# Kernel optimization log

Hardware: AMD Instinct MI355X
Metric: run time of the kernel (lower is better)

## Reference

```python
import jax, jax.numpy as jnp
import numpy as np

N_NODES = 10000
N_EDGES = 320000
K_HOPS = 3
IN_CH = 128
OUT_CH = 128


def setup_inputs() -> dict:
    key = jax.random.key(0)
    k1, k2, k3, k4, k5 = jax.random.split(key, 5)
    h = jax.random.normal(k1, (N_NODES, IN_CH), dtype=jnp.float32)
    X = jax.random.normal(k2, (N_EDGES, K_HOPS), dtype=jnp.float32)
    edge_index = jax.random.randint(k3, (2, N_EDGES), 0, N_NODES, dtype=jnp.int64)
    batch_node = jax.random.uniform(k4, (N_NODES,), dtype=jnp.float32)
    # glorot init for weight, zeros for bias (matches reset_parameters)
    stdv = np.sqrt(6.0 / (IN_CH + OUT_CH))
    weight = jax.random.uniform(k5, (K_HOPS, IN_CH, OUT_CH), dtype=jnp.float32,
                                minval=-stdv, maxval=stdv)
    bias = jnp.zeros((OUT_CH,), dtype=jnp.float32)
    return {"h": h, "X": X, "edge_index": edge_index,
            "batch_node": batch_node, "weight": weight, "bias": bias}


def reference(h, X, edge_index, batch_node, weight, bias):
    # Original builds dense A[k, src, dst] = X[e, k] (zeros elsewhere), then
    # res = A @ h @ weight, max over k, + bias. We honor the sparsity:
    # agg[src, k, :] = sum_e X[e, k] * h[dst[e], :]  (sparse A @ h per hop k)
    n = batch_node.shape[0]
    src = edge_index[0]
    dst = edge_index[1]
    msg = X[:, :, None] * h[dst][:, None, :]                 # [E, K, in]
    agg = jax.ops.segment_sum(msg, src, num_segments=n)      # [N, K, in]
    res = jnp.einsum('nki,kio->kno', agg, weight)            # [K, N, out]
    out = res.max(axis=0) + bias                             # [N, out]
    return out
```

## Files before the change

kernel.cpp:

```cpp
#include <hip/hip_runtime.h>

#define N_NODES 10000
#define N_EDGES 320000
#define K_HOPS  3
#define CH      128
#define NBF     8
#define ROWP    136
#define SUBSLOT 44
#define SLOT    88
#define SEPAD   96
#define CSTRIDE 16

#define EDGE_BLKS 1250
#define HCV_BLKS  1250
#define WCV_BLKS  192

typedef __attribute__((ext_vector_type(8))) short  frag8;
typedef __attribute__((ext_vector_type(4))) float  floatx4;

__device__ inline unsigned short f2bf(float x) {
    union { float f; unsigned u; } v; v.f = x;
    unsigned r = v.u + 0x7fff + ((v.u >> 16) & 1);
    return (unsigned short)(r >> 16);
}

__global__ __launch_bounds__(256) void prep_fill_kernel(
    const float* __restrict__ h, const float* __restrict__ X,
    const int* __restrict__ ei, const float* __restrict__ W,
    unsigned short* __restrict__ hb, unsigned short* __restrict__ WT,
    int* __restrict__ cursor, uint2* __restrict__ edata)
{
    int b = blockIdx.x;
    if (b < EDGE_BLKS) {
        int e = b * 256 + threadIdx.x;
        int src = ei[e];
        int dst = ei[N_EDGES + e];
        int j = e & 1;
        int r = atomicAdd(cursor + (2 * src + j) * CSTRIDE, 1);
        if (r < SUBSLOT) {
            uint2 rec;
            rec.x = (unsigned)f2bf(X[e * K_HOPS + 0])
                  | ((unsigned)f2bf(X[e * K_HOPS + 1]) << 16);
            rec.y = (unsigned)f2bf(X[e * K_HOPS + 2])
                  | ((unsigned)dst << 16);
            edata[(size_t)src * SLOT + j * SUBSLOT + r] = rec;
        }
    } else if (b < EDGE_BLKS + HCV_BLKS) {
        int tid = (b - EDGE_BLKS) * 256 + threadIdx.x;
        float4 v = *(const float4*)(h + (size_t)tid * 4);
        ushort4 p;
        p.x = f2bf(v.x); p.y = f2bf(v.y); p.z = f2bf(v.z); p.w = f2bf(v.w);
        *(ushort4*)(hb + (size_t)tid * 4) = p;
    } else {
        int tid = (b - EDGE_BLKS - HCV_BLKS) * 256 + threadIdx.x;
        int i = tid & 127;
        int o = (tid >> 7) & 127;
        int k = tid >> 14;
        WT[tid] = f2bf(W[((size_t)k * CH + i) * CH + o]);
    }
}

__device__ inline void estep(uint2 er, uint2 q, float (&a)[12]) {
    float x0 = __uint_as_float(er.x << 16);
    float x1 = __uint_as_float(er.x & 0xffff0000u);
    float x2 = __uint_as_float(er.y << 16);
    float h0 = __uint_as_float(q.x << 16);
    float h1 = __uint_as_float(q.x & 0xffff0000u);
    float h2 = __uint_as_float(q.y << 16);
    float h3 = __uint_as_float(q.y & 0xffff0000u);
    a[0] = fmaf(x0, h0, a[0]); a[1]  = fmaf(x0, h1, a[1]);
    a[2] = fmaf(x0, h2, a[2]); a[3]  = fmaf(x0, h3, a[3]);
    a[4] = fmaf(x1, h0, a[4]); a[5]  = fmaf(x1, h1, a[5]);
    a[6] = fmaf(x1, h2, a[6]); a[7]  = fmaf(x1, h3, a[7]);
    a[8] = fmaf(x2, h0, a[8]); a[9]  = fmaf(x2, h1, a[9]);
    a[10]= fmaf(x2, h2, a[10]); a[11]= fmaf(x2, h3, a[11]);
}

__global__ __launch_bounds__(256, 5) void fused_kernel(
    const unsigned short* __restrict__ hb,
    const uint2*          __restrict__ edata,
    const int*            __restrict__ cursor,
    const unsigned short* __restrict__ WT,
    const float*          __restrict__ bias,
    float*                __restrict__ out)
{
    __shared__ unsigned short sA[K_HOPS][16][ROWP];
    __shared__ uint2 sE[NBF][SEPAD];
    const int node0 = blockIdx.x * NBF;
    const int t    = threadIdx.x;
    const int w    = t >> 6;
    const int lane = t & 63;
    const int half = lane >> 5;
    const int cq   = (lane & 31) * 4;

    const int rA = 2 * w, rB = rA + 1;
    const int nA = node0 + rA, nB = node0 + rB;
    int a0 = __builtin_amdgcn_readfirstlane(min(cursor[(2 * nA + 0) * CSTRIDE], SUBSLOT));
    int a1 = __builtin_amdgcn_readfirstlane(min(cursor[(2 * nA + 1) * CSTRIDE], SUBSLOT));
    int b0 = __builtin_amdgcn_readfirstlane(min(cursor[(2 * nB + 0) * CSTRIDE], SUBSLOT));
    int b1 = __builtin_amdgcn_readfirstlane(min(cursor[(2 * nB + 1) * CSTRIDE], SUBSLOT));
    const int cA = a0 + a1, cB = b0 + b1;
    const uint2* eA = edata + (size_t)nA * SLOT;
    const uint2* eB = edata + (size_t)nB * SLOT;

    if (lane < a0) sE[rA][lane]      = eA[lane];
    if (lane < a1) sE[rA][a0 + lane] = eA[SUBSLOT + lane];
    if (lane < b0) sE[rB][lane]      = eB[lane];
    if (lane < b1) sE[rB][b0 + lane] = eB[SUBSLOT + lane];
    {
        uint2 zz; zz.x = 0u; zz.y = 0u;
        int zA0 = cA + lane, zA1 = cA + 64 + lane;
        if (zA0 < SEPAD) sE[rA][zA0] = zz;
        if (zA1 < SEPAD) sE[rA][zA1] = zz;
        int zB0 = cB + lane, zB1 = cB + 64 + lane;
        if (zB0 < SEPAD) sE[rB][zB0] = zz;
        if (zB1 < SEPAD) sE[rB][zB1] = zz;
    }

    float accA[12], accB[12];
#pragma unroll
    for (int i = 0; i < 12; ++i) { accA[i] = 0.f; accB[i] = 0.f; }

    const int gmax = (max(cA, cB) + 15) >> 4;
    for (int g = 0; g < gmax; ++g) {
        const int s = g * 8;
        uint2 erA[8], qA[8];
#pragma unroll
        for (int k = 0; k < 8; ++k) erA[k] = sE[rA][2 * (s + k) + half];
#pragma unroll
        for (int k = 0; k < 8; ++k)
            qA[k] = *(const uint2*)(hb + ((size_t)(erA[k].y >> 16) << 7) + cq);
#pragma unroll
        for (int k = 0; k < 8; ++k) estep(erA[k], qA[k], accA);

        uint2 erB[8], qB[8];
#pragma unroll
        for (int k = 0; k < 8; ++k) erB[k] = sE[rB][2 * (s + k) + half];
#pragma unroll
        for (int k = 0; k < 8; ++k)
            qB[k] = *(const uint2*)(hb + ((size_t)(erB[k].y >> 16) << 7) + cq);
#pragma unroll
        for (int k = 0; k < 8; ++k) estep(erB[k], qB[k], accB);
    }

#pragma unroll
    for (int i = 0; i < 12; ++i) {
        accA[i] += __shfl_xor(accA[i], 32, 64);
        accB[i] += __shfl_xor(accB[i], 32, 64);
    }

    if (half == 0) {
#pragma unroll
        for (int hop = 0; hop < K_HOPS; ++hop) {
            ushort4 pA, pB;
            pA.x = f2bf(accA[4 * hop + 0]); pA.y = f2bf(accA[4 * hop + 1]);
            pA.z = f2bf(accA[4 * hop + 2]); pA.w = f2bf(accA[4 * hop + 3]);
            pB.x = f2bf(accB[4 * hop + 0]); pB.y = f2bf(accB[4 * hop + 1]);
            pB.z = f2bf(accB[4 * hop + 2]); pB.w = f2bf(accB[4 * hop + 3]);
            *(ushort4*)&sA[hop][rA][cq] = pA;
            *(ushort4*)&sA[hop][rB][cq] = pB;
        }
    }
    __syncthreads();

    const int col  = lane & 15;
    const int quad = lane >> 4;
    const int ob0 = 32 * w, ob1 = ob0 + 16;

    floatx4 m0a = {-3.4e38f, -3.4e38f, -3.4e38f, -3.4e38f};
    floatx4 m0b = {-3.4e38f, -3.4e38f, -3.4e38f, -3.4e38f};
#pragma unroll
    for (int hop = 0; hop < K_HOPS; ++hop) {
        frag8 af[4];
        const unsigned short* arow = &sA[hop][col][quad * 8];
#pragma unroll
        for (int kt = 0; kt < 4; ++kt) af[kt] = *(const frag8*)(arow + kt * 32);

        const unsigned short* bp0 = WT + ((size_t)hop * CH + ob0 + col) * CH + quad * 8;
        floatx4 cv0 = {0.f, 0.f, 0.f, 0.f};
#pragma unroll
        for (int kt = 0; kt < 4; ++kt) {
            frag8 bf = *(const frag8*)(bp0 + kt * 32);
            cv0 = __builtin_amdgcn_mfma_f32_16x16x32_bf16(af[kt], bf, cv0, 0, 0, 0);
        }
#pragma unroll
        for (int r = 0; r < 4; ++r) m0a[r] = fmaxf(m0a[r], cv0[r]);

        const unsigned short* bp1 = WT + ((size_t)hop * CH + ob1 + col) * CH + quad * 8;
        floatx4 cv1 = {0.f, 0.f, 0.f, 0.f};
#pragma unroll
        for (int kt = 0; kt < 4; ++kt) {
            frag8 bf = *(const frag8*)(bp1 + kt * 32);
            cv1 = __builtin_amdgcn_mfma_f32_16x16x32_bf16(af[kt], bf, cv1, 0, 0, 0);
        }
#pragma unroll
        for (int r = 0; r < 4; ++r) m0b[r] = fmaxf(m0b[r], cv1[r]);
    }

    if (quad < 2) {
        const float bv0 = bias[ob0 + col];
        const float bv1 = bias[ob1 + col];
#pragma unroll
        for (int r = 0; r < 4; ++r) {
            int row = quad * 4 + r;
            out[(size_t)(node0 + row) * CH + ob0 + col] = m0a[r] + bv0;
            out[(size_t)(node0 + row) * CH + ob1 + col] = m0b[r] + bv1;
        }
    }
}

extern "C" void kernel_launch(void* const* d_in, const int* in_sizes, int n_in,
                              void* d_out, int out_size, void* d_ws, size_t ws_size,
                              hipStream_t stream) {
    const float* h    = (const float*)d_in[0];
    const float* X    = (const float*)d_in[1];
    const int*   ei   = (const int*)  d_in[2];
    const float* W    = (const float*)d_in[4];
    const float* bias = (const float*)d_in[5];
    float*       out  = (float*)d_out;

    char* ws = (char*)d_ws;
    int* cursor = (int*)ws;                        ws += (size_t)N_NODES * 2 * CSTRIDE * sizeof(int);
    unsigned short* hb = (unsigned short*)ws;      ws += (size_t)N_NODES * CH * sizeof(unsigned short);
    unsigned short* WT = (unsigned short*)ws;      ws += (size_t)K_HOPS * CH * CH * sizeof(unsigned short);
    uint2* edata = (uint2*)ws;

    hipMemsetAsync(cursor, 0, (size_t)N_NODES * 2 * CSTRIDE * sizeof(int), stream);

    prep_fill_kernel<<<EDGE_BLKS + HCV_BLKS + WCV_BLKS, 256, 0, stream>>>(
        h, X, ei, W, hb, WT, cursor, edata);
    fused_kernel<<<(N_NODES + NBF - 1) / NBF, 256, 0, stream>>>(
        hb, edata, cursor, WT, bias, out);
}
```

Baseline: 112.7 us.

## Merge memset, prep and fused kernels into one cooperative persistent kernel

Replaces the memset plus two kernel launches with a single cooperative kernel that zeroes the cursors, fills the edge buckets, converts h and W to bf16, and then runs the aggregation and MFMA stage over node groups in a grid-stride loop. Grid-wide syncs separate the phases. The aim is to remove launch and inter-kernel gaps. In exchange it adds grid-barrier cost, lowers occupancy to 4 blocks per CU, and makes each persistent block handle several node groups serially, which may reduce latency hiding in the gather-bound phase.

```diff
diff --git a/kernel.cpp b/kernel.cpp
--- a/kernel.cpp
+++ b/kernel.cpp
@@ -1,19 +1,21 @@
 #include <hip/hip_runtime.h>
+#include <hip/hip_cooperative_groups.h>
+
+namespace cg = cooperative_groups;
 
 #define N_NODES 10000
 #define N_EDGES 320000
 #define K_HOPS  3
 #define CH      128
 #define NBF     8
+#define NGROUPS (N_NODES / NBF)
 #define ROWP    136
 #define SUBSLOT 44
 #define SLOT    88
 #define SEPAD   96
 #define CSTRIDE 16
-
-#define EDGE_BLKS 1250
-#define HCV_BLKS  1250
-#define WCV_BLKS  192
+#define CUR_INTS (N_NODES * 2 * CSTRIDE)
+#define W_ELEMS (K_HOPS * CH * CH)
 
 typedef __attribute__((ext_vector_type(8))) short  frag8;
 typedef __attribute__((ext_vector_type(4))) float  floatx4;
@@ -22,42 +24,6 @@
     union { float f; unsigned u; } v; v.f = x;
     unsigned r = v.u + 0x7fff + ((v.u >> 16) & 1);
     return (unsigned short)(r >> 16);
-}
-
-__global__ __launch_bounds__(256) void prep_fill_kernel(
-    const float* __restrict__ h, const float* __restrict__ X,
-    const int* __restrict__ ei, const float* __restrict__ W,
-    unsigned short* __restrict__ hb, unsigned short* __restrict__ WT,
-    int* __restrict__ cursor, uint2* __restrict__ edata)
-{
-    int b = blockIdx.x;
-    if (b < EDGE_BLKS) {
-        int e = b * 256 + threadIdx.x;
-        int src = ei[e];
-        int dst = ei[N_EDGES + e];
-        int j = e & 1;
-        int r = atomicAdd(cursor + (2 * src + j) * CSTRIDE, 1);
-        if (r < SUBSLOT) {
-            uint2 rec;
-            rec.x = (unsigned)f2bf(X[e * K_HOPS + 0])
-                  | ((unsigned)f2bf(X[e * K_HOPS + 1]) << 16);
-            rec.y = (unsigned)f2bf(X[e * K_HOPS + 2])
-                  | ((unsigned)dst << 16);
-            edata[(size_t)src * SLOT + j * SUBSLOT + r] = rec;
-        }
-    } else if (b < EDGE_BLKS + HCV_BLKS) {
-        int tid = (b - EDGE_BLKS) * 256 + threadIdx.x;
-        float4 v = *(const float4*)(h + (size_t)tid * 4);
-        ushort4 p;
-        p.x = f2bf(v.x); p.y = f2bf(v.y); p.z = f2bf(v.z); p.w = f2bf(v.w);
-        *(ushort4*)(hb + (size_t)tid * 4) = p;
-    } else {
-        int tid = (b - EDGE_BLKS - HCV_BLKS) * 256 + threadIdx.x;
-        int i = tid & 127;
-        int o = (tid >> 7) & 127;
-        int k = tid >> 14;
-        WT[tid] = f2bf(W[((size_t)k * CH + i) * CH + o]);
-    }
 }
 
 __device__ inline void estep(uint2 er, uint2 q, float (&a)[12]) {
@@ -76,135 +42,174 @@
     a[10]= fmaf(x2, h2, a[10]); a[11]= fmaf(x2, h3, a[11]);
 }
 
-__global__ __launch_bounds__(256, 5) void fused_kernel(
-    const unsigned short* __restrict__ hb,
-    const uint2*          __restrict__ edata,
-    const int*            __restrict__ cursor,
-    const unsigned short* __restrict__ WT,
-    const float*          __restrict__ bias,
-    float*                __restrict__ out)
+__global__ __launch_bounds__(256, 4) void mega_kernel(
+    const float* __restrict__ h, const float* __restrict__ X,
+    const int* __restrict__ ei, const float* __restrict__ W,
+    const float* __restrict__ bias,
+    unsigned short* __restrict__ hb, unsigned short* __restrict__ WT,
+    int* __restrict__ cursor, uint2* __restrict__ edata,
+    float* __restrict__ out)
 {
     __shared__ unsigned short sA[K_HOPS][16][ROWP];
     __shared__ uint2 sE[NBF][SEPAD];
-    const int node0 = blockIdx.x * NBF;
-    const int t    = threadIdx.x;
+
+    cg::grid_group grid = cg::this_grid();
+    const int t      = threadIdx.x;
+    const int gtid   = blockIdx.x * 256 + t;
+    const int stride = gridDim.x * 256;
+
+    for (int i = gtid; i < CUR_INTS; i += stride) cursor[i] = 0;
+    __threadfence();
+    grid.sync();
+
+    for (int e = gtid; e < N_EDGES; e += stride) {
+        int src = ei[e];
+        int dst = ei[N_EDGES + e];
+        int j = e & 1;
+        int r = atomicAdd(cursor + (2 * src + j) * CSTRIDE, 1);
+        if (r < SUBSLOT) {
+            uint2 rec;
+            rec.x = (unsigned)f2bf(X[e * K_HOPS + 0])
+                  | ((unsigned)f2bf(X[e * K_HOPS + 1]) << 16);
+            rec.y = (unsigned)f2bf(X[e * K_HOPS + 2])
+                  | ((unsigned)dst << 16);
+            edata[(size_t)src * SLOT + j * SUBSLOT + r] = rec;
+        }
+        float4 v = *(const float4*)(h + (size_t)e * 4);
+        ushort4 p;
+        p.x = f2bf(v.x); p.y = f2bf(v.y); p.z = f2bf(v.z); p.w = f2bf(v.w);
+        *(ushort4*)(hb + (size_t)e * 4) = p;
+        if (e < W_ELEMS) {
+            int ic = e & 127;
+            int oc = (e >> 7) & 127;
+            int k  = e >> 14;
+            WT[e] = f2bf(W[((size_t)k * CH + ic) * CH + oc]);
+        }
+    }
+    __threadfence();
+    grid.sync();
+
     const int w    = t >> 6;
     const int lane = t & 63;
     const int half = lane >> 5;
     const int cq   = (lane & 31) * 4;
-
-    const int rA = 2 * w, rB = rA + 1;
-    const int nA = node0 + rA, nB = node0 + rB;
-    int a0 = __builtin_amdgcn_readfirstlane(min(cursor[(2 * nA + 0) * CSTRIDE], SUBSLOT));
-    int a1 = __builtin_amdgcn_readfirstlane(min(cursor[(2 * nA + 1) * CSTRIDE], SUBSLOT));
-    int b0 = __builtin_amdgcn_readfirstlane(min(cursor[(2 * nB + 0) * CSTRIDE], SUBSLOT));
-    int b1 = __builtin_amdgcn_readfirstlane(min(cursor[(2 * nB + 1) * CSTRIDE], SUBSLOT));
-    const int cA = a0 + a1, cB = b0 + b1;
-    const uint2* eA = edata + (size_t)nA * SLOT;
-    const uint2* eB = edata + (size_t)nB * SLOT;
-
-    if (lane < a0) sE[rA][lane]      = eA[lane];
-    if (lane < a1) sE[rA][a0 + lane] = eA[SUBSLOT + lane];
-    if (lane < b0) sE[rB][lane]      = eB[lane];
-    if (lane < b1) sE[rB][b0 + lane] = eB[SUBSLOT + lane];
-    {
-        uint2 zz; zz.x = 0u; zz.y = 0u;
-        int zA0 = cA + lane, zA1 = cA + 64 + lane;
-        if (zA0 < SEPAD) sE[rA][zA0] = zz;
-        if (zA1 < SEPAD) sE[rA][zA1] = zz;
-        int zB0 = cB + lane, zB1 = cB + 64 + lane;
-        if (zB0 < SEPAD) sE[rB][zB0] = zz;
-        if (zB1 < SEPAD) sE[rB][zB1] = zz;
-    }
-
-    float accA[12], accB[12];
-#pragma unroll
-    for (int i = 0; i < 12; ++i) { accA[i] = 0.f; accB[i] = 0.f; }
-
-    const int gmax = (max(cA, cB) + 15) >> 4;
-    for (int g = 0; g < gmax; ++g) {
-        const int s = g * 8;
-        uint2 erA[8], qA[8];
-#pragma unroll
-        for (int k = 0; k < 8; ++k) erA[k] = sE[rA][2 * (s + k) + half];
-#pragma unroll
-        for (int k = 0; k < 8; ++k)
-            qA[k] = *(const uint2*)(hb + ((size_t)(erA[k].y >> 16) << 7) + cq);
-#pragma unroll
-        for (int k = 0; k < 8; ++k) estep(erA[k], qA[k], accA);
-
-        uint2 erB[8], qB[8];
-#pragma unroll
-        for (int k = 0; k < 8; ++k) erB[k] = sE[rB][2 * (s + k) + half];
-#pragma unroll
-        for (int k = 0; k < 8; ++k)
-            qB[k] = *(const uint2*)(hb + ((size_t)(erB[k].y >> 16) << 7) + cq);
-#pragma unroll
-        for (int k = 0; k < 8; ++k) estep(erB[k], qB[k], accB);
-    }
-
-#pragma unroll
-    for (int i = 0; i < 12; ++i) {
-        accA[i] += __shfl_xor(accA[i], 32, 64);
-        accB[i] += __shfl_xor(accB[i], 32, 64);
-    }
-
-    if (half == 0) {
-#pragma unroll
-        for (int hop = 0; hop < K_HOPS; ++hop) {
-            ushort4 pA, pB;
-            pA.x = f2bf(accA[4 * hop + 0]); pA.y = f2bf(accA[4 * hop + 1]);
-            pA.z = f2bf(accA[4 * hop + 2]); pA.w = f2bf(accA[4 * hop + 3]);
-            pB.x = f2bf(accB[4 * hop + 0]); pB.y = f2bf(accB[4 * hop + 1]);
-            pB.z = f2bf(accB[4 * hop + 2]); pB.w = f2bf(accB[4 * hop + 3]);
-            *(ushort4*)&sA[hop][rA][cq] = pA;
-            *(ushort4*)&sA[hop][rB][cq] = pB;
-        }
-    }
-    __syncthreads();
-
     const int col  = lane & 15;
     const int quad = lane >> 4;
-    const int ob0 = 32 * w, ob1 = ob0 + 16;
-
-    floatx4 m0a = {-3.4e38f, -3.4e38f, -3.4e38f, -3.4e38f};
-    floatx4 m0b = {-3.4e38f, -3.4e38f, -3.4e38f, -3.4e38f};
-#pragma unroll
-    for (int hop = 0; hop < K_HOPS; ++hop) {
-        frag8 af[4];
-        const unsigned short* arow = &sA[hop][col][quad * 8];
-#pragma unroll
-        for (int kt = 0; kt < 4; ++kt) af[kt] = *(const frag8*)(arow + kt * 32);
-
-        const unsigned short* bp0 = WT + ((size_t)hop * CH + ob0 + col) * CH + quad * 8;
-        floatx4 cv0 = {0.f, 0.f, 0.f, 0.f};
-#pragma unroll
-        for (int kt = 0; kt < 4; ++kt) {
-            frag8 bf = *(const frag8*)(bp0 + kt * 32);
-            cv0 = __builtin_amdgcn_mfma_f32_16x16x32_bf16(af[kt], bf, cv0, 0, 0, 0);
-        }
-#pragma unroll
-        for (int r = 0; r < 4; ++r) m0a[r] = fmaxf(m0a[r], cv0[r]);
-
-        const unsigned short* bp1 = WT + ((size_t)hop * CH + ob1 + col) * CH + quad * 8;
-        floatx4 cv1 = {0.f, 0.f, 0.f, 0.f};
-#pragma unroll
-        for (int kt = 0; kt < 4; ++kt) {
-            frag8 bf = *(const frag8*)(bp1 + kt * 32);
-            cv1 = __builtin_amdgcn_mfma_f32_16x16x32_bf16(af[kt], bf, cv1, 0, 0, 0);
-        }
-#pragma unroll
-        for (int r = 0; r < 4; ++r) m0b[r] = fmaxf(m0b[r], cv1[r]);
-    }
-
-    if (quad < 2) {
-        const float bv0 = bias[ob0 + col];
-        const float bv1 = bias[ob1 + col];
-#pragma unroll
-        for (int r = 0; r < 4; ++r) {
-            int row = quad * 4 + r;
-            out[(size_t)(node0 + row) * CH + ob0 + col] = m0a[r] + bv0;
-            out[(size_t)(node0 + row) * CH + ob1 + col] = m0b[r] + bv1;
+    const int ob0  = 32 * w, ob1 = ob0 + 16;
+
+    for (int grp = blockIdx.x; grp < NGROUPS; grp += gridDim.x) {
+        const int node0 = grp * NBF;
+        const int rA = 2 * w, rB = rA + 1;
+        const int nA = node0 + rA, nB = node0 + rB;
+        int a0 = __builtin_amdgcn_readfirstlane(min(cursor[(2 * nA + 0) * CSTRIDE], SUBSLOT));
+        int a1 = __builtin_amdgcn_readfirstlane(min(cursor[(2 * nA + 1) * CSTRIDE], SUBSLOT));
+        int b0 = __builtin_amdgcn_readfirstlane(min(cursor[(2 * nB + 0) * CSTRIDE], SUBSLOT));
+        int b1 = __builtin_amdgcn_readfirstlane(min(cursor[(2 * nB + 1) * CSTRIDE], SUBSLOT));
+        const int cA = a0 + a1, cB = b0 + b1;
+        const uint2* eA = edata + (size_t)nA * SLOT;
+        const uint2* eB = edata + (size_t)nB * SLOT;
+
+        if (lane < a0) sE[rA][lane]      = eA[lane];
+        if (lane < a1) sE[rA][a0 + lane] = eA[SUBSLOT + lane];
+        if (lane < b0) sE[rB][lane]      = eB[lane];
+        if (lane < b1) sE[rB][b0 + lane] = eB[SUBSLOT + lane];
+        {
+            uint2 zz; zz.x = 0u; zz.y = 0u;
+            int zA0 = cA + lane, zA1 = cA + 64 + lane;
+            if (zA0 < SEPAD) sE[rA][zA0] = zz;
+            if (zA1 < SEPAD) sE[rA][zA1] = zz;
+            int zB0 = cB + lane, zB1 = cB + 64 + lane;
+            if (zB0 < SEPAD) sE[rB][zB0] = zz;
+            if (zB1 < SEPAD) sE[rB][zB1] = zz;
+        }
+
+        float accA[12], accB[12];
+#pragma unroll
+        for (int i = 0; i < 12; ++i) { accA[i] = 0.f; accB[i] = 0.f; }
+
+        const int gmax = (max(cA, cB) + 15) >> 4;
+        for (int g = 0; g < gmax; ++g) {
+            const int s = g * 8;
+            uint2 erA[8], qA[8];
+#pragma unroll
+            for (int k = 0; k < 8; ++k) erA[k] = sE[rA][2 * (s + k) + half];
+#pragma unroll
+            for (int k = 0; k < 8; ++k)
+                qA[k] = *(const uint2*)(hb + ((size_t)(erA[k].y >> 16) << 7) + cq);
+#pragma unroll
+            for (int k = 0; k < 8; ++k) estep(erA[k], qA[k], accA);
+
+            uint2 erB[8], qB[8];
+#pragma unroll
+            for (int k = 0; k < 8; ++k) erB[k] = sE[rB][2 * (s + k) + half];
+#pragma unroll
+            for (int k = 0; k < 8; ++k)
+                qB[k] = *(const uint2*)(hb + ((size_t)(erB[k].y >> 16) << 7) + cq);
+#pragma unroll
+            for (int k = 0; k < 8; ++k) estep(erB[k], qB[k], accB);
+        }
+
+#pragma unroll
+        for (int i = 0; i < 12; ++i) {
+            accA[i] += __shfl_xor(accA[i], 32, 64);
+            accB[i] += __shfl_xor(accB[i], 32, 64);
+        }
+
+        __syncthreads();
+
+        if (half == 0) {
+#pragma unroll
+            for (int hop = 0; hop < K_HOPS; ++hop) {
+                ushort4 pA, pB;
+                pA.x = f2bf(accA[4 * hop + 0]); pA.y = f2bf(accA[4 * hop + 1]);
+                pA.z = f2bf(accA[4 * hop + 2]); pA.w = f2bf(accA[4 * hop + 3]);
+                pB.x = f2bf(accB[4 * hop + 0]); pB.y = f2bf(accB[4 * hop + 1]);
+                pB.z = f2bf(accB[4 * hop + 2]); pB.w = f2bf(accB[4 * hop + 3]);
+                *(ushort4*)&sA[hop][rA][cq] = pA;
+                *(ushort4*)&sA[hop][rB][cq] = pB;
+            }
+        }
+        __syncthreads();
+
+        floatx4 m0a = {-3.4e38f, -3.4e38f, -3.4e38f, -3.4e38f};
+        floatx4 m0b = {-3.4e38f, -3.4e38f, -3.4e38f, -3.4e38f};
+#pragma unroll
+        for (int hop = 0; hop < K_HOPS; ++hop) {
+            frag8 af[4];
+            const unsigned short* arow = &sA[hop][col][quad * 8];
+#pragma unroll
+            for (int kt = 0; kt < 4; ++kt) af[kt] = *(const frag8*)(arow + kt * 32);
+
+            const unsigned short* bp0 = WT + ((size_t)hop * CH + ob0 + col) * CH + quad * 8;
+            floatx4 cv0 = {0.f, 0.f, 0.f, 0.f};
+#pragma unroll
+            for (int kt = 0; kt < 4; ++kt) {
+                frag8 bf = *(const frag8*)(bp0 + kt * 32);
+                cv0 = __builtin_amdgcn_mfma_f32_16x16x32_bf16(af[kt], bf, cv0, 0, 0, 0);
+            }
+#pragma unroll
+            for (int r = 0; r < 4; ++r) m0a[r] = fmaxf(m0a[r], cv0[r]);
+
+            const unsigned short* bp1 = WT + ((size_t)hop * CH + ob1 + col) * CH + quad * 8;
+            floatx4 cv1 = {0.f, 0.f, 0.f, 0.f};
+#pragma unroll
+            for (int kt = 0; kt < 4; ++kt) {
+                frag8 bf = *(const frag8*)(bp1 + kt * 32);
+                cv1 = __builtin_amdgcn_mfma_f32_16x16x32_bf16(af[kt], bf, cv1, 0, 0, 0);
+            }
+#pragma unroll
+            for (int r = 0; r < 4; ++r) m0b[r] = fmaxf(m0b[r], cv1[r]);
+        }
+
+        if (quad < 2) {
+            const float bv0 = bias[ob0 + col];
+            const float bv1 = bias[ob1 + col];
+#pragma unroll
+            for (int r = 0; r < 4; ++r) {
+                int row = quad * 4 + r;
+                out[(size_t)(node0 + row) * CH + ob0 + col] = m0a[r] + bv0;
+                out[(size_t)(node0 + row) * CH + ob1 + col] = m0b[r] + bv1;
+            }
         }
     }
 }
@@ -220,15 +225,28 @@
     float*       out  = (float*)d_out;
 
     char* ws = (char*)d_ws;
-    int* cursor = (int*)ws;                        ws += (size_t)N_NODES * 2 * CSTRIDE * sizeof(int);
+    int* cursor = (int*)ws;                        ws += (size_t)CUR_INTS * sizeof(int);
     unsigned short* hb = (unsigned short*)ws;      ws += (size_t)N_NODES * CH * sizeof(unsigned short);
-    unsigned short* WT = (unsigned short*)ws;      ws += (size_t)K_HOPS * CH * CH * sizeof(unsigned short);
+    unsigned short* WT = (unsigned short*)ws;      ws += (size_t)W_ELEMS * sizeof(unsigned short);
     uint2* edata = (uint2*)ws;
 
-    hipMemsetAsync(cursor, 0, (size_t)N_NODES * 2 * CSTRIDE * sizeof(int), stream);
-
-    prep_fill_kernel<<<EDGE_BLKS + HCV_BLKS + WCV_BLKS, 256, 0, stream>>>(
-        h, X, ei, W, hb, WT, cursor, edata);
-    fused_kernel<<<(N_NODES + NBF - 1) / NBF, 256, 0, stream>>>(
-        hb, edata, cursor, WT, bias, out);
-}
+    static int gblocks = 0;
+    if (gblocks == 0) {
+        int nb = 0;
+        if (hipOccupancyMaxActiveBlocksPerMultiprocessor(
+                &nb, (const void*)mega_kernel, 256, 0) != hipSuccess || nb < 1)
+            nb = 3;
+        int ncu = 0;
+        if (hipDeviceGetAttribute(&ncu, hipDeviceAttributeMultiprocessorCount, 0)
+                != hipSuccess || ncu < 1)
+            ncu = 256;
+        long cap = (long)nb * (long)ncu;
+        gblocks = (int)(cap < NGROUPS ? cap : NGROUPS);
+    }
+
+    void* args[] = { (void*)&h, (void*)&X, (void*)&ei, (void*)&W, (void*)&bias,
+                     (void*)&hb, (void*)&WT, (void*)&cursor, (void*)&edata,
+                     (void*)&out };
+    hipLaunchCooperativeKernel((const void*)mega_kernel, dim3(gblocks), dim3(256),
+                               args, 0, stream);
+}
```

Result: slower. 318.7 us (+182.8%).
